# Optimization experiments

Measured on AMD Instinct MI355X. Metric: run time of the kernel, lower is better.

Reference implementation:

```python
import jax, jax.numpy as jnp
import numpy as np

B, C, H, W = 4, 512, 64, 64
INTER = 64  # C // channel_stride


def setup_inputs() -> dict:
    key = jax.random.key(0)
    ks = jax.random.split(key, 5)
    s = 0.02  # small init scale for numerical stability of softmax logits
    return {
        "inputs": jax.random.normal(ks[0], (B, C, H, W), dtype=jnp.float32),
        "Wq": jax.random.normal(ks[1], (INTER, C), dtype=jnp.float32) * s,
        "bq": jnp.zeros((INTER,), dtype=jnp.float32),
        "Wk": jax.random.normal(ks[2], (INTER, C), dtype=jnp.float32) * s,
        "bk": jnp.zeros((INTER,), dtype=jnp.float32),
        "Wv": jax.random.normal(ks[3], (C, C), dtype=jnp.float32) * s,
        "bv": jnp.zeros((C,), dtype=jnp.float32),
        "gamma": jax.random.normal(ks[4], (1,), dtype=jnp.float32),
    }


def reference(inputs, Wq, bq, Wk, bk, Wv, bv, gamma):
    b, c, h, w = inputs.shape
    n = h * w
    x = inputs.reshape(b, c, n)  # (B, C, N)
    # 1x1 convs == per-pixel linear projections
    q = jnp.einsum('dc,bcn->bnd', Wq, x) + bq            # (B, N, d)
    k = jnp.einsum('dc,bcn->bdn', Wk, x) + bk[:, None]   # (B, d, N)
    v = jnp.einsum('oc,bcn->bon', Wv, x) + bv[:, None]   # (B, O, N)
    # affinity: (B, Nq, Nk), softmax over keys (last dim), no scaling (as in source)
    affinity = jax.nn.softmax(jnp.einsum('bnd,bdm->bnm', q, k), axis=-1)
    # note: torch does bmm(value, affinity) -> out[b,o,m] = sum_j v[b,o,j] * A[b,j,m]
    out = jnp.einsum('bon,bnm->bom', v, affinity)        # (B, O, N)
    return gamma * out.reshape(b, -1, h, w) + inputs
```

## Files before the change

### kernel.cpp

```cpp
#include <hip/hip_runtime.h>
#include <stdint.h>

typedef __attribute__((ext_vector_type(8))) short short8;
typedef __attribute__((ext_vector_type(4))) float f32x4;
typedef __attribute__((ext_vector_type(8))) unsigned short u16x8;
typedef __attribute__((ext_vector_type(4))) unsigned short u16x4;
typedef __attribute__((ext_vector_type(2))) unsigned short u16x2;
typedef unsigned short u16;

#define NPIX 4096
#define CCH  512
#define DD   64


__device__ inline float b2f(u16 h){
  union { unsigned int i; float f; } u; u.i = ((unsigned int)h) << 16; return u.f;
}
__device__ inline u16 f2b(float f){
  union { float f; unsigned int i; } u; u.f = f;
  return (u16)((u.i + 0x7fffu + ((u.i >> 16) & 1u)) >> 16);
}
__device__ inline void gl2lds16(const void* g, void* l){
  __builtin_amdgcn_global_load_lds((const __attribute__((address_space(1))) unsigned int*)g,
                                   (__attribute__((address_space(3))) unsigned int*)l, 16, 0, 0);
}
__device__ inline f32x4 mfma16(short8 a, short8 b, f32x4 c){
  return __builtin_amdgcn_mfma_f32_16x16x32_bf16(a, b, c, 0, 0, 0);
}

__global__ __launch_bounds__(256) void k0_transpose(const float* __restrict__ x,
    u16* __restrict__ xT, const float* __restrict__ Wq, const float* __restrict__ Wk,
    const float* __restrict__ Wv, u16* __restrict__ Wqkb, u16* __restrict__ Wvb){
  if (blockIdx.z == 4){
    int bid = blockIdx.x * 8 + blockIdx.y;
    for (int r = 0; r < 3; ++r){
      int i = (r * 512 + bid) * 256 + threadIdx.x;
      if (i < 65536){
        int row = i >> 9, col = i & 511;
        float v = (row < 64) ? Wq[(row << 9) + col] : Wk[((row - 64) << 9) + col];
        Wqkb[(row << 9) + (col ^ ((row & 7) << 3))] = f2b(v);
      } else if (i < 327680){
        int j = i - 65536;
        int row = j >> 9, col = j & 511;
        Wvb[(row << 9) + (col ^ ((row & 7) << 3))] = f2b(Wv[j]);
      }
    }
    return;
  }
  __shared__ u16 tile[64][66];
  const int b = blockIdx.z;
  const int n0 = blockIdx.x * 64, c0 = blockIdx.y * 64;
  const float* xb = x + ((size_t)b * CCH + c0) * NPIX + n0;
  #pragma unroll
  for (int r = 0; r < 16; ++r){
    int id = r * 256 + threadIdx.x;
    int cc = id >> 6, nn = id & 63;
    tile[nn][cc] = f2b(xb[(size_t)cc * NPIX + nn]);
  }
  __syncthreads();
  u16* xTb = xT + ((size_t)b * NPIX + n0) * CCH + c0;
  #pragma unroll
  for (int r = 0; r < 8; ++r){
    int id = r * 256 + threadIdx.x;
    int nn = id >> 5, c2 = id & 31;
    int colp = (2 * c2) ^ ((nn & 7) << 3);
    *(u16x2*)(xTb + (size_t)nn * CCH + colp) = *(const u16x2*)&tile[nn][2 * c2];
  }
}

__global__ __launch_bounds__(256) void k1_qk(const u16* __restrict__ xT,
    const u16* __restrict__ Wqk, const float* __restrict__ bq,
    const float* __restrict__ bk, u16* __restrict__ Qb, u16* __restrict__ Kb){
  __shared__ __align__(16) u16 As[128*64];
  __shared__ __align__(16) u16 Bs[128*64];
  const int b  = blockIdx.z;
  const int n0 = blockIdx.x * 128;
  const u16* Ab = xT + ((size_t)b * NPIX + n0) * CCH;
  const int t = threadIdx.x, wave = t >> 6, lane = t & 63, q = lane >> 4, l16 = lane & 15;
  const int wr = (wave >> 1) * 64, wc = (wave & 1) * 64;
  const int sw = l16 & 7;
  f32x4 acc[4][4];
  #pragma unroll
  for (int i = 0; i < 4; ++i)
    #pragma unroll
    for (int j = 0; j < 4; ++j) acc[i][j] = (f32x4){0.f,0.f,0.f,0.f};

  for (int k0 = 0; k0 < CCH; k0 += 64){
    __syncthreads();
    #pragma unroll
    for (int r = 0; r < 4; ++r){
      int id = r * 256 + t;
      int row = id >> 3, ko = (id & 7) << 3;
      gl2lds16(Ab + (size_t)row * CCH + k0 + ko, &As[id * 8]);
      gl2lds16(Wqk + (size_t)row * CCH + k0 + ko, &Bs[id * 8]);
    }
    __syncthreads();
    #pragma unroll
    for (int s = 0; s < 2; ++s){
      const int ca = ((s*4 + q) ^ sw) << 3;
      short8 af[4], bfr[4];
      #pragma unroll
      for (int i = 0; i < 4; ++i){
        af[i]  = *(const short8*)&As[(wr + i*16 + l16)*64 + ca];
        bfr[i] = *(const short8*)&Bs[(wc + i*16 + l16)*64 + ca];
      }
      #pragma unroll
      for (int i = 0; i < 4; ++i)
        #pragma unroll
        for (int j = 0; j < 4; ++j)
          acc[i][j] = mfma16(af[i], bfr[j], acc[i][j]);
    }
  }
  #pragma unroll
  for (int i = 0; i < 4; ++i){
    #pragma unroll
    for (int j = 0; j < 4; ++j){
      int col = wc + j*16 + l16;
      #pragma unroll
      for (int r2 = 0; r2 < 4; ++r2){
        int n = n0 + wr + i*16 + q*4 + r2;
        int sw8 = (n & 7) << 3;
        float v = acc[i][j][r2];
        if (col < 64) Qb[((size_t)b * NPIX + n) * DD + (col ^ sw8)]        = f2b(v + bq[col]);
        else          Kb[((size_t)b * NPIX + n) * DD + ((col - 64) ^ sw8)] = f2b(v + bk[col - 64]);
      }
    }
  }
}

__global__ __launch_bounds__(256) void k2_v(const u16* __restrict__ xT,
    const u16* __restrict__ Wvb, const float* __restrict__ bv, u16* __restrict__ Vb){
  __shared__ __align__(16) u16 As[128*64];
  __shared__ __align__(16) u16 Bs[128*64];
  const int b  = blockIdx.z;
  const int n0 = blockIdx.x * 128;
  const int o0 = blockIdx.y * 128;
  const u16* Ab = Wvb + (size_t)o0 * CCH;
  const u16* Bb = xT + ((size_t)b * NPIX + n0) * CCH;
  const int t = threadIdx.x, wave = t >> 6, lane = t & 63, q = lane >> 4, l16 = lane & 15;
  const int wr = (wave >> 1) * 64, wc = (wave & 1) * 64;
  const int sw = l16 & 7;
  f32x4 acc[4][4];
  #pragma unroll
  for (int i = 0; i < 4; ++i)
    #pragma unroll
    for (int j = 0; j < 4; ++j) acc[i][j] = (f32x4){0.f,0.f,0.f,0.f};

  for (int k0 = 0; k0 < CCH; k0 += 64){
    __syncthreads();
    #pragma unroll
    for (int r = 0; r < 4; ++r){
      int id = r * 256 + t;
      int row = id >> 3, ko = (id & 7) << 3;
      gl2lds16(Ab + (size_t)row * CCH + k0 + ko, &As[id * 8]);
      gl2lds16(Bb + (size_t)row * CCH + k0 + ko, &Bs[id * 8]);
    }
    __syncthreads();
    #pragma unroll
    for (int s = 0; s < 2; ++s){
      const int ca = ((s*4 + q) ^ sw) << 3;
      short8 af[4], bfr[4];
      #pragma unroll
      for (int i = 0; i < 4; ++i){
        af[i]  = *(const short8*)&As[(wr + i*16 + l16)*64 + ca];
        bfr[i] = *(const short8*)&Bs[(wc + i*16 + l16)*64 + ca];
      }
      #pragma unroll
      for (int i = 0; i < 4; ++i)
        #pragma unroll
        for (int j = 0; j < 4; ++j)
          acc[i][j] = mfma16(af[i], bfr[j], acc[i][j]);
    }
  }
  #pragma unroll
  for (int i = 0; i < 4; ++i){
    #pragma unroll
    for (int j = 0; j < 4; ++j){
      int n = n0 + wc + j*16 + l16;
      #pragma unroll
      for (int r2 = 0; r2 < 4; ++r2){
        int o = o0 + wr + i*16 + q*4 + r2;
        int np = n ^ ((o & 7) << 3);
        Vb[((size_t)b * CCH + o) * NPIX + np] = f2b(acc[i][j][r2] + bv[o]);
      }
    }
  }
}

__global__ __launch_bounds__(256) void k3_logits(const u16* __restrict__ Qb,
    const u16* __restrict__ Kb, u16* __restrict__ E, float* __restrict__ Z, int b0){
  __shared__ __align__(16) u16 smem[128*136];
  u16* As = smem;
  u16* Bs = smem + 128*64;
  const int bloc = blockIdx.z, b = b0 + bloc;
  const int n0 = blockIdx.x * 128;
  const int m0 = blockIdx.y * 128;
  const u16* Ab = Kb + ((size_t)b * NPIX + m0) * DD;
  const u16* Bb = Qb + ((size_t)b * NPIX + n0) * DD;
  const int t = threadIdx.x, wave = t >> 6, lane = t & 63, q = lane >> 4, l16 = lane & 15;
  const int wr = (wave >> 1) * 64, wc = (wave & 1) * 64;
  const int sw = l16 & 7;
  f32x4 acc[4][4];
  #pragma unroll
  for (int i = 0; i < 4; ++i)
    #pragma unroll
    for (int j = 0; j < 4; ++j) acc[i][j] = (f32x4){0.f,0.f,0.f,0.f};

  #pragma unroll
  for (int r = 0; r < 4; ++r){
    int id = r * 256 + t;
    int row = id >> 3, ko = (id & 7) << 3;
    gl2lds16(Ab + row * DD + ko, &As[id * 8]);
    gl2lds16(Bb + row * DD + ko, &Bs[id * 8]);
  }
  __syncthreads();
  #pragma unroll
  for (int s = 0; s < 2; ++s){
    const int ca = ((s*4 + q) ^ sw) << 3;
    short8 af[4], bfr[4];
    #pragma unroll
    for (int i = 0; i < 4; ++i){
      af[i]  = *(const short8*)&As[(wr + i*16 + l16)*64 + ca];
      bfr[i] = *(const short8*)&Bs[(wc + i*16 + l16)*64 + ca];
    }
    #pragma unroll
    for (int i = 0; i < 4; ++i)
      #pragma unroll
      for (int j = 0; j < 4; ++j)
        acc[i][j] = mfma16(af[i], bfr[j], acc[i][j]);
  }
  __syncthreads();
  u16* tile = smem;
  float colsum[4] = {0.f, 0.f, 0.f, 0.f};
  #pragma unroll
  for (int i = 0; i < 4; ++i){
    #pragma unroll
    for (int j = 0; j < 4; ++j){
      #pragma unroll
      for (int r2 = 0; r2 < 4; ++r2){
        int mrow = wr + i*16 + q*4 + r2;
        int ncol = wc + j*16 + l16;
        float l = fminf(fmaxf(acc[i][j][r2], -60.f), 30.f);
        float e = __expf(l);
        tile[mrow * 136 + ncol] = f2b(e);
        colsum[j] += e;
      }
    }
  }
  #pragma unroll
  for (int j = 0; j < 4; ++j){
    float v = colsum[j];
    v += __shfl_xor(v, 16, 64);
    v += __shfl_xor(v, 32, 64);
    if (q == 0) atomicAdd(&Z[(size_t)b * NPIX + n0 + wc + j*16 + l16], v);
  }
  __syncthreads();
  u16* Eb = E + (size_t)bloc * NPIX * NPIX;
  #pragma unroll
  for (int r = 0; r < 8; ++r){
    int id = r * 256 + t;
    int row = id >> 4, chunk = id & 15;
    int g = chunk >> 3, c3 = chunk & 7;
    int colp = g * 64 + ((c3 ^ (row & 7)) << 3);
    *(u16x8*)(Eb + (size_t)(m0 + row) * NPIX + n0 + colp) =
        *(const u16x8*)&tile[row * 136 + chunk * 8];
  }
}

__global__ __launch_bounds__(256) void k3b_scale(u16* __restrict__ Vb,
    const float* __restrict__ Z, const float* __restrict__ gm, int b0){
  size_t i4  = ((size_t)blockIdx.x * 256 + threadIdx.x) * 4;
  size_t off = ((size_t)b0 << 21) + i4;
  int b = (int)(off >> 21);
  int o = (int)((off >> 12) & 511);
  int np = (int)(off & (NPIX - 1));
  int nl = np ^ ((o & 7) << 3);
  float g = gm[0];
  u16x4 vv = *(const u16x4*)(Vb + off);
  f32x4 zz = *(const f32x4*)(Z + ((size_t)b << 12) + nl);
  u16x4 r;
  #pragma unroll
  for (int k = 0; k < 4; ++k) r[k] = f2b(g * b2f(vv[k]) / fmaxf(zz[k], 1e-20f));
  *(u16x4*)(Vb + off) = r;
}

__global__ __launch_bounds__(256, 2) void k4_out(const u16* __restrict__ Vs,
    const u16* __restrict__ E, const float* __restrict__ xin,
    float* __restrict__ outp, int b0){
  __shared__ __align__(16) u16 smem[33792];
  u16* As = smem;
  const int bloc = blockIdx.z, b = b0 + bloc;
  const int m0 = blockIdx.x * 128;
  const int o0 = blockIdx.y * 128;
  const u16* Ab = Vs + ((size_t)b * CCH + o0) * NPIX;
  const u16* Bb = E + (size_t)bloc * NPIX * NPIX + (size_t)m0 * NPIX;
  const int t = threadIdx.x, wave = t >> 6, lane = t & 63, q = lane >> 4, l16 = lane & 15;
  const int grp = wave >> 1;
  const int br  = (wave & 1) * 64;
  const int sw = l16 & 7;
  const int ca = ((grp * 4 + q) ^ sw) << 3;
  const u16* bp = Bb + (size_t)(br + l16) * NPIX + (size_t)ca;

  auto stageA = [&](int kt, int slot){
    const int k0 = kt << 6;
    u16* dst = As + slot * (128*64);
    #pragma unroll
    for (int r = 0; r < 4; ++r){
      int id = r * 256 + t;
      gl2lds16(Ab + (size_t)(id >> 3) * NPIX + (k0 + ((id & 7) << 3)), dst + id * 8);
    }
  };

  f32x4 acc[8][4];
  #pragma unroll
  for (int i = 0; i < 8; ++i)
    #pragma unroll
    for (int j = 0; j < 4; ++j) acc[i][j] = (f32x4){0.f,0.f,0.f,0.f};

  short8 bfrA[4], bfrB[4];
  stageA(0, 0);
  #pragma unroll
  for (int j = 0; j < 4; ++j)
    bfrA[j] = *(const short8*)(bp + (size_t)j * 16 * NPIX);
  asm volatile("s_waitcnt vmcnt(0)" ::: "memory");
  __builtin_amdgcn_sched_barrier(0);
  __builtin_amdgcn_s_barrier();

  for (int kt = 0; kt < NPIX / 64; kt += 2){
    {
      short8 af[8];
      #pragma unroll
      for (int i = 0; i < 8; ++i) af[i] = *(const short8*)&As[(i*16 + l16)*64 + ca];
      #pragma unroll
      for (int j = 0; j < 4; ++j)
        bfrB[j] = *(const short8*)(bp + (size_t)j * 16 * NPIX + (size_t)((kt + 1) << 6));
      stageA(kt + 1, 1);
      asm volatile("s_waitcnt lgkmcnt(0)" ::: "memory");
      __builtin_amdgcn_sched_barrier(0);
      __builtin_amdgcn_s_setprio(1);
      #pragma unroll
      for (int i = 0; i < 8; ++i)
        #pragma unroll
        for (int j = 0; j < 4; ++j)
          acc[i][j] = mfma16(af[i], bfrA[j], acc[i][j]);
      __builtin_amdgcn_s_setprio(0);
      asm volatile("s_waitcnt vmcnt(0)" ::: "memory");
      __builtin_amdgcn_sched_barrier(0);
      __builtin_amdgcn_s_barrier();
    }
    {
      const bool pf = (kt + 2) < NPIX / 64;
      short8 af[8];
      #pragma unroll
      for (int i = 0; i < 8; ++i)
        af[i] = *(const short8*)&As[128*64 + (i*16 + l16)*64 + ca];
      if (pf){
        #pragma unroll
        for (int j = 0; j < 4; ++j)
          bfrA[j] = *(const short8*)(bp + (size_t)j * 16 * NPIX + (size_t)((kt + 2) << 6));
        stageA(kt + 2, 0);
      }
      asm volatile("s_waitcnt lgkmcnt(0)" ::: "memory");
      __builtin_amdgcn_sched_barrier(0);
      __builtin_amdgcn_s_setprio(1);
      #pragma unroll
      for (int i = 0; i < 8; ++i)
        #pragma unroll
        for (int j = 0; j < 4; ++j)
          acc[i][j] = mfma16(af[i], bfrB[j], acc[i][j]);
      __builtin_amdgcn_s_setprio(0);
      asm volatile("s_waitcnt vmcnt(0)" ::: "memory");
      __builtin_amdgcn_sched_barrier(0);
      __builtin_amdgcn_s_barrier();
    }
  }

  float* red = (float*)smem;
  if (grp == 1){
    #pragma unroll
    for (int i = 0; i < 8; ++i)
      #pragma unroll
      for (int j = 0; j < 4; ++j)
        *(f32x4*)&red[(size_t)(br + j*16 + l16) * 132 + i*16 + q*4] = acc[i][j];
  }
  __syncthreads();
  if (grp == 0){
    const float* xb = xin + (size_t)b * CCH * NPIX;
    float* ob = outp + (size_t)b * CCH * NPIX;
    #pragma unroll
    for (int i = 0; i < 8; ++i){
      #pragma unroll
      for (int j = 0; j < 4; ++j){
        f32x4 p = *(const f32x4*)&red[(size_t)(br + j*16 + l16) * 132 + i*16 + q*4];
        int m = m0 + br + j*16 + l16;
        #pragma unroll
        for (int r2 = 0; r2 < 4; ++r2){
          int o = o0 + i*16 + q*4 + r2;
          size_t idx = (size_t)o * NPIX + m;
          ob[idx] = acc[i][j][r2] + p[r2] + xb[idx];
        }
      }
    }
  }
}

extern "C" void kernel_launch(void* const* d_in, const int* in_sizes, int n_in,
                              void* d_out, int out_size, void* d_ws, size_t ws_size,
                              hipStream_t stream){
  (void)in_sizes; (void)n_in; (void)out_size;
  const float* x  = (const float*)d_in[0];
  const float* Wq = (const float*)d_in[1];
  const float* bq = (const float*)d_in[2];
  const float* Wk = (const float*)d_in[3];
  const float* bk = (const float*)d_in[4];
  const float* Wv = (const float*)d_in[5];
  const float* bv = (const float*)d_in[6];
  const float* gm = (const float*)d_in[7];
  float* outp = (float*)d_out;

  char* ws = (char*)d_ws;
  u16*  Qb   = (u16*)(ws + 0);
  u16*  Kb   = (u16*)(ws + 2097152);
  u16*  Vb   = (u16*)(ws + 4194304);
  float* Z   = (float*)(ws + 20971520);
  u16*  Wqkb = (u16*)(ws + 21037056);
  u16*  Wvb  = (u16*)(ws + 21168128);
  u16*  xT   = (u16*)(ws + 21692416);
  u16*  E    = (u16*)(ws + 21692416);

  const size_t ebytes = (size_t)NPIX * NPIX * 2;
  const size_t base   = 21692416;
  if (ws_size < base + ebytes){
    return;
  }
  int NB = 1;
  if (ws_size >= base + 4 * ebytes) NB = 4;
  else if (ws_size >= base + 2 * ebytes) NB = 2;

  hipMemsetAsync(Z, 0, (size_t)4 * NPIX * sizeof(float), stream);
  k0_transpose<<<dim3(64, 8, 5), 256, 0, stream>>>(x, xT, Wq, Wk, Wv, Wqkb, Wvb);
  k1_qk<<<dim3(32, 1, 4), 256, 0, stream>>>(xT, Wqkb, bq, bk, Qb, Kb);
  k2_v<<<dim3(32, 4, 4), 256, 0, stream>>>(xT, Wvb, bv, Vb);
  for (int b0 = 0; b0 < 4; b0 += NB){
    int nb = NB; if (b0 + nb > 4) nb = 4 - b0;
    k3_logits<<<dim3(32, 32, nb), 256, 0, stream>>>(Qb, Kb, E, Z, b0);
    k3b_scale<<<dim3(nb * 2048), 256, 0, stream>>>(Vb, Z, gm, b0);
    k4_out<<<dim3(32, 4, nb), 256, 0, stream>>>(Vb, E, x, outp, b0);
  }
}
```

Measured before the change: 237.4 us.

## Double k4_out output-channel tile to 256 with 512 threads to reuse E

k4_out now computes a 256x128 output tile with 8 waves instead of 128x128 with 4 waves. Each block reads its slice of the large affinity matrix E once for twice as many output channels, which is meant to halve E traffic from global memory. The A-tile staging is issued before the B register loads and the wait is relaxed to vmcnt(4), so the B prefetch can stay in flight across the barrier. The cost is a larger LDS footprint, a two-pass cross-group reduction in the epilogue, and possibly higher register pressure or lower occupancy.

```diff
diff --git a/kernel.cpp b/kernel.cpp
--- a/kernel.cpp
+++ b/kernel.cpp
@@ -284,29 +284,30 @@
   *(u16x4*)(Vb + off) = r;
 }
 
-__global__ __launch_bounds__(256, 2) void k4_out(const u16* __restrict__ Vs,
+__global__ __launch_bounds__(512, 2) void k4_out(const u16* __restrict__ Vs,
     const u16* __restrict__ E, const float* __restrict__ xin,
     float* __restrict__ outp, int b0){
   __shared__ __align__(16) u16 smem[33792];
   u16* As = smem;
   const int bloc = blockIdx.z, b = b0 + bloc;
   const int m0 = blockIdx.x * 128;
-  const int o0 = blockIdx.y * 128;
+  const int o0 = blockIdx.y * 256;
   const u16* Ab = Vs + ((size_t)b * CCH + o0) * NPIX;
   const u16* Bb = E + (size_t)bloc * NPIX * NPIX + (size_t)m0 * NPIX;
   const int t = threadIdx.x, wave = t >> 6, lane = t & 63, q = lane >> 4, l16 = lane & 15;
-  const int grp = wave >> 1;
-  const int br  = (wave & 1) * 64;
+  const int grp = (wave >> 2) & 1;
+  const int wo  = (wave >> 1) & 1;
+  const int wm  = wave & 1;
   const int sw = l16 & 7;
   const int ca = ((grp * 4 + q) ^ sw) << 3;
-  const u16* bp = Bb + (size_t)(br + l16) * NPIX + (size_t)ca;
+  const u16* bp = Bb + (size_t)(wm * 64 + l16) * NPIX + (size_t)ca;
 
   auto stageA = [&](int kt, int slot){
     const int k0 = kt << 6;
-    u16* dst = As + slot * (128*64);
+    u16* dst = As + slot * (256*64);
     #pragma unroll
     for (int r = 0; r < 4; ++r){
-      int id = r * 256 + t;
+      int id = r * 512 + t;
       gl2lds16(Ab + (size_t)(id >> 3) * NPIX + (k0 + ((id & 7) << 3)), dst + id * 8);
     }
   };
@@ -326,15 +327,17 @@
   __builtin_amdgcn_sched_barrier(0);
   __builtin_amdgcn_s_barrier();
 
+  const int aoff = wo * 128;
   for (int kt = 0; kt < NPIX / 64; kt += 2){
     {
       short8 af[8];
       #pragma unroll
-      for (int i = 0; i < 8; ++i) af[i] = *(const short8*)&As[(i*16 + l16)*64 + ca];
+      for (int i = 0; i < 8; ++i)
+        af[i] = *(const short8*)&As[(aoff + i*16 + l16)*64 + ca];
+      stageA(kt + 1, 1);
       #pragma unroll
       for (int j = 0; j < 4; ++j)
         bfrB[j] = *(const short8*)(bp + (size_t)j * 16 * NPIX + (size_t)((kt + 1) << 6));
-      stageA(kt + 1, 1);
       asm volatile("s_waitcnt lgkmcnt(0)" ::: "memory");
       __builtin_amdgcn_sched_barrier(0);
       __builtin_amdgcn_s_setprio(1);
@@ -344,7 +347,7 @@
         for (int j = 0; j < 4; ++j)
           acc[i][j] = mfma16(af[i], bfrA[j], acc[i][j]);
       __builtin_amdgcn_s_setprio(0);
-      asm volatile("s_waitcnt vmcnt(0)" ::: "memory");
+      asm volatile("s_waitcnt vmcnt(4)" ::: "memory");
       __builtin_amdgcn_sched_barrier(0);
       __builtin_amdgcn_s_barrier();
     }
@@ -353,12 +356,12 @@
       short8 af[8];
       #pragma unroll
       for (int i = 0; i < 8; ++i)
-        af[i] = *(const short8*)&As[128*64 + (i*16 + l16)*64 + ca];
+        af[i] = *(const short8*)&As[256*64 + (aoff + i*16 + l16)*64 + ca];
       if (pf){
+        stageA(kt + 2, 0);
         #pragma unroll
         for (int j = 0; j < 4; ++j)
           bfrA[j] = *(const short8*)(bp + (size_t)j * 16 * NPIX + (size_t)((kt + 2) << 6));
-        stageA(kt + 2, 0);
       }
       asm volatile("s_waitcnt lgkmcnt(0)" ::: "memory");
       __builtin_amdgcn_sched_barrier(0);
@@ -369,38 +372,43 @@
         for (int j = 0; j < 4; ++j)
           acc[i][j] = mfma16(af[i], bfrB[j], acc[i][j]);
       __builtin_amdgcn_s_setprio(0);
-      asm volatile("s_waitcnt vmcnt(0)" ::: "memory");
+      if (pf){ asm volatile("s_waitcnt vmcnt(4)" ::: "memory"); }
+      else   { asm volatile("s_waitcnt vmcnt(0)" ::: "memory"); }
       __builtin_amdgcn_sched_barrier(0);
       __builtin_amdgcn_s_barrier();
     }
   }
 
   float* red = (float*)smem;
-  if (grp == 1){
-    #pragma unroll
-    for (int i = 0; i < 8; ++i)
-      #pragma unroll
-      for (int j = 0; j < 4; ++j)
-        *(f32x4*)&red[(size_t)(br + j*16 + l16) * 132 + i*16 + q*4] = acc[i][j];
-  }
-  __syncthreads();
-  if (grp == 0){
-    const float* xb = xin + (size_t)b * CCH * NPIX;
-    float* ob = outp + (size_t)b * CCH * NPIX;
-    #pragma unroll
-    for (int i = 0; i < 8; ++i){
-      #pragma unroll
-      for (int j = 0; j < 4; ++j){
-        f32x4 p = *(const f32x4*)&red[(size_t)(br + j*16 + l16) * 132 + i*16 + q*4];
-        int m = m0 + br + j*16 + l16;
-        #pragma unroll
-        for (int r2 = 0; r2 < 4; ++r2){
-          int o = o0 + i*16 + q*4 + r2;
-          size_t idx = (size_t)o * NPIX + m;
-          ob[idx] = acc[i][j][r2] + p[r2] + xb[idx];
+  const float* xb = xin + (size_t)b * CCH * NPIX;
+  float* ob = outp + (size_t)b * CCH * NPIX;
+  #pragma unroll
+  for (int r = 0; r < 2; ++r){
+    if (grp == 1 && wo == r){
+      #pragma unroll
+      for (int i = 0; i < 8; ++i)
+        #pragma unroll
+        for (int j = 0; j < 4; ++j)
+          *(f32x4*)&red[(size_t)(wm*64 + j*16 + l16) * 132 + i*16 + q*4] = acc[i][j];
+    }
+    __syncthreads();
+    if (grp == 0 && wo == r){
+      #pragma unroll
+      for (int i = 0; i < 8; ++i){
+        #pragma unroll
+        for (int j = 0; j < 4; ++j){
+          f32x4 p = *(const f32x4*)&red[(size_t)(wm*64 + j*16 + l16) * 132 + i*16 + q*4];
+          int m = m0 + wm*64 + j*16 + l16;
+          #pragma unroll
+          for (int r2 = 0; r2 < 4; ++r2){
+            int o = o0 + r*128 + i*16 + q*4 + r2;
+            size_t idx = (size_t)o * NPIX + m;
+            ob[idx] = acc[i][j][r2] + p[r2] + xb[idx];
+          }
         }
       }
     }
+    __syncthreads();
   }
 }
 
@@ -445,6 +453,6 @@
     int nb = NB; if (b0 + nb > 4) nb = 4 - b0;
     k3_logits<<<dim3(32, 32, nb), 256, 0, stream>>>(Qb, Kb, E, Z, b0);
     k3b_scale<<<dim3(nb * 2048), 256, 0, stream>>>(Vb, Z, gm, b0);
-    k4_out<<<dim3(32, 4, nb), 256, 0, stream>>>(Vb, E, x, outp, b0);
-  }
-}
+    k4_out<<<dim3(32, 2, nb), 512, 0, stream>>>(Vb, E, x, outp, b0);
+  }
+}
```

New measurement: 241.5 us. About the same (+1.7%).
